# Performance work log

Hardware: AMD Instinct MI355X
Metric: run time of the kernel (lower is better)

Reference implementation:

```python
import jax, jax.numpy as jnp
import numpy as np

B, L, DM, DI, N = 8, 2048, 512, 768, 8  # batch, seq, d_model, d_inner=int(1.5*512), d_state


def setup_inputs() -> dict:
    key = jax.random.key(0)
    ks = jax.random.split(key, 8)
    g = lambda k, shape, sc=1.0: (jax.random.normal(k, shape, jnp.float32) * sc)
    return {
        "x": g(ks[0], (B, L, DM)),
        "W_in": g(ks[1], (DM, 2 * DI), 0.02),    # in_proj weight (stored in->out)
        "A_log": g(ks[2], (DI, N)),               # nn.Parameter(randn)
        "D_param": g(ks[3], (DI,)),               # skip-connection D
        "W_x": g(ks[4], (DI, N), 0.02),           # x_proj weight
        "W_dt": g(ks[5], (N, DI), 0.02),          # dt_proj weight
        "b_dt": jnp.zeros((DI,), jnp.float32),    # dt_proj bias
        "W_out": g(ks[6], (DI, DM), 0.02),        # out_proj weight
    }


def reference(x, W_in, A_log, D_param, W_x, W_dt, b_dt, W_out):
    xz = x @ W_in                                  # (B,L,2*DI)
    d_inner = W_in.shape[1] // 2
    x_ssm, z = xz[..., :d_inner], xz[..., d_inner:]
    x_ssm = jax.nn.silu(x_ssm)                     # (B,L,DI)
    A = -jnp.exp(A_log.astype(jnp.float32))        # (DI,N)
    delta = jax.nn.softplus((x_ssm @ W_x) @ W_dt + b_dt)  # (B,L,DI)

    n_state = A.shape[-1]

    def step(h, inp):
        xt, dt = inp                               # each (B,DI)
        dA = jnp.exp(dt[..., None] * A)            # (B,DI,N)
        h = dA * h + dt[..., None] * xt[..., None]
        y = jnp.sum(h, axis=-1) + D_param * xt     # (B,DI)
        return h, y

    h0 = jnp.zeros((x.shape[0], d_inner, n_state), x_ssm.dtype)
    xs = (jnp.swapaxes(x_ssm, 0, 1), jnp.swapaxes(delta, 0, 1))  # (L,B,DI)
    _, ys = jax.lax.scan(step, h0, xs)             # ys: (L,B,DI)
    y = jnp.swapaxes(ys, 0, 1)                     # (B,L,DI)
    y = y * jax.nn.silu(z)
    return y @ W_out                               # (B,L,DM)
```

## Files before the change

kernel.cpp:

```cpp
#include <hip/hip_runtime.h>

typedef unsigned short bfu;
typedef __attribute__((ext_vector_type(8))) short short8;
typedef __attribute__((ext_vector_type(4))) float f32x4;

__device__ __forceinline__ float bf2f(bfu u){
  union { unsigned int i; float f; } v; v.i = ((unsigned int)u) << 16; return v.f;
}
__device__ __forceinline__ bfu f2bf(float f){
  union { float f; unsigned int i; } v; v.f = f;
  unsigned int r = (v.i + 0x7FFFu + ((v.i >> 16) & 1u)) >> 16;
  return (bfu)r;
}
__device__ __forceinline__ float fexp2(float x){ return __builtin_amdgcn_exp2f(x); }
__device__ __forceinline__ float flog2(float x){ return __builtin_amdgcn_logf(x); }
__device__ __forceinline__ float softplusf(float x){
  float t = fexp2(-fabsf(x) * 1.44269504088896f);
  return fmaxf(x, 0.f) + 0.69314718055995f * flog2(1.f + t);
}
__device__ __forceinline__ void gload16(const bfu* g, bfu* l){
  __builtin_amdgcn_global_load_lds((const __attribute__((address_space(1))) unsigned int*)g,
                                   (__attribute__((address_space(3))) unsigned int*)l, 16, 0, 0);
}

__global__ __launch_bounds__(256) void cvt_all_kernel(const float* __restrict__ x, bfu* __restrict__ x_bf,
                                                      const float* __restrict__ W_in, const float* __restrict__ W_out,
                                                      const float* __restrict__ W_x,
                                                      bfu* __restrict__ WinT, bfu* __restrict__ WoutT,
                                                      float* __restrict__ WxT){
  __shared__ float T[32][33];
  const int bid = blockIdx.x;
  const int tid = threadIdx.x;
  if (bid < 8192){
    int g = bid * 256 + tid;
    float4 v = ((const float4*)x)[g];
    ushort4 o;
    o.x = f2bf(v.x); o.y = f2bf(v.y); o.z = f2bf(v.z); o.w = f2bf(v.w);
    ((ushort4*)x_bf)[g] = o;
    return;
  }
  const int lr = tid >> 3;
  const int lc = tid & 7;
  if (bid < 8960){
    int ti = bid - 8192;
    int r0 = (ti & 15) * 32, c0 = (ti >> 4) * 32;
    float4 v = *(const float4*)(W_in + (size_t)(r0 + lr) * 1536 + c0 + lc * 4);
    T[lr][lc * 4 + 0] = v.x; T[lr][lc * 4 + 1] = v.y;
    T[lr][lc * 4 + 2] = v.z; T[lr][lc * 4 + 3] = v.w;
    __syncthreads();
    ushort4 o;
    o.x = f2bf(T[lc * 4 + 0][lr]); o.y = f2bf(T[lc * 4 + 1][lr]);
    o.z = f2bf(T[lc * 4 + 2][lr]); o.w = f2bf(T[lc * 4 + 3][lr]);
    *(ushort4*)(WinT + (size_t)(c0 + lr) * 512 + r0 + lc * 4) = o;
  } else if (bid < 9344){
    int ti = bid - 8960;
    int r0 = (ti % 24) * 32, c0 = (ti / 24) * 32;
    float4 v = *(const float4*)(W_out + (size_t)(r0 + lr) * 512 + c0 + lc * 4);
    T[lr][lc * 4 + 0] = v.x; T[lr][lc * 4 + 1] = v.y;
    T[lr][lc * 4 + 2] = v.z; T[lr][lc * 4 + 3] = v.w;
    __syncthreads();
    ushort4 o;
    o.x = f2bf(T[lc * 4 + 0][lr]); o.y = f2bf(T[lc * 4 + 1][lr]);
    o.z = f2bf(T[lc * 4 + 2][lr]); o.w = f2bf(T[lc * 4 + 3][lr]);
    *(ushort4*)(WoutT + (size_t)(c0 + lr) * 768 + r0 + lc * 4) = o;
  } else {
    int h = (bid - 9344) * 256 + tid;
    int n = h / 768, k = h % 768;
    WxT[h] = W_x[(size_t)k * 8 + n];
  }
}

template<int EPI, int BM, int KK>
__global__ __launch_bounds__(BM * 2)
void gemm_sb(const bfu* __restrict__ Amat, const bfu* __restrict__ Bt,
             void* __restrict__ out0, void* __restrict__ out1,
             int NBN, int N)
{
  constexpr int BN = 128;
  constexpr int THREADS = BM * 2;
  constexpr int RPI = THREADS / 8;
  __shared__ bfu As[BM * 64];
  __shared__ bfu Bs[BN * 64];
  const int tid  = threadIdx.x;
  const int lane = tid & 63;
  const int w    = tid >> 6;
  const int wr   = w >> 1, wc = w & 1;

  const int cpx = gridDim.x >> 3;
  const int id  = blockIdx.x;
  const int nid = (id & 7) * cpx + (id >> 3);
  const int bn  = nid % NBN;
  const int bm  = nid / NBN;

  const int srow = tid >> 3;
  const int scol = ((tid & 7) ^ (srow & 7)) * 8;
  const bfu* gA = Amat + ((size_t)(bm * BM + srow)) * KK + scol;
  const bfu* gB = Bt   + ((size_t)(bn * BN + srow)) * KK + scol;
  bfu* lA = As + srow * 64 + (tid & 7) * 8;
  bfu* lB = Bs + srow * 64 + (tid & 7) * 8;

  f32x4 acc[4][4];
  #pragma unroll
  for (int i = 0; i < 4; i++)
    #pragma unroll
    for (int j = 0; j < 4; j++)
      #pragma unroll
      for (int r = 0; r < 4; r++) acc[i][j][r] = 0.f;

  for (int k0 = 0; k0 < KK; k0 += 64){
    #pragma unroll
    for (int i = 0; i < BM / RPI; i++)
      gload16(gA + (size_t)(i * RPI) * KK + k0, lA + i * RPI * 64);
    #pragma unroll
    for (int j = 0; j < BN / RPI; j++)
      gload16(gB + (size_t)(j * RPI) * KK + k0, lB + j * RPI * 64);
    __syncthreads();

    #pragma unroll
    for (int kk = 0; kk < 2; kk++){
      short8 a[4], b[4];
      const int sA = ((kk * 4 + (lane >> 4)) ^ (lane & 7)) * 8;
      #pragma unroll
      for (int m = 0; m < 4; m++){
        int r = wr * 64 + m * 16 + (lane & 15);
        a[m] = *(const short8*)&As[r * 64 + sA];
      }
      #pragma unroll
      for (int n = 0; n < 4; n++){
        int r = wc * 64 + n * 16 + (lane & 15);
        b[n] = *(const short8*)&Bs[r * 64 + sA];
      }
      #pragma unroll
      for (int m = 0; m < 4; m++)
        #pragma unroll
        for (int n = 0; n < 4; n++)
          acc[m][n] = __builtin_amdgcn_mfma_f32_16x16x32_bf16(a[m], b[n], acc[m][n], 0, 0, 0);
    }
    __syncthreads();
  }

  #pragma unroll
  for (int m = 0; m < 4; m++){
    #pragma unroll
    for (int n = 0; n < 4; n++){
      const int row0 = bm * BM + wr * 64 + m * 16 + (lane >> 4) * 4;
      const int col  = bn * BN + wc * 64 + n * 16 + (lane & 15);
      #pragma unroll
      for (int r = 0; r < 4; r++){
        float v = acc[m][n][r];
        int row = row0 + r;
        if (EPI == 0){
          float s = v / (1.f + __expf(-v));
          if (col < 768) ((bfu*)out0)[(size_t)row * 768 + col]         = f2bf(s);
          else           ((bfu*)out1)[(size_t)row * 768 + (col - 768)] = f2bf(s);
        } else {
          ((float*)out0)[(size_t)row * N + col] = v;
        }
      }
    }
  }
}

__global__ __launch_bounds__(256) void u_kernel(const bfu* __restrict__ xssm, const float* __restrict__ WxT,
                                                float* __restrict__ u){
  int wid = threadIdx.x >> 6, lane = threadIdx.x & 63;
  int row = blockIdx.x * 4 + wid;
  const bfu* xr = xssm + (size_t)row * 768;
  float acc[8];
  #pragma unroll
  for (int n = 0; n < 8; n++) acc[n] = 0.f;
  #pragma unroll
  for (int i = 0; i < 3; i++){
    int kb = i * 256 + lane * 4;
    ushort4 xq = *(const ushort4*)(xr + kb);
    float x0 = bf2f(xq.x), x1 = bf2f(xq.y), x2 = bf2f(xq.z), x3 = bf2f(xq.w);
    #pragma unroll
    for (int n = 0; n < 8; n++){
      float4 wv = *(const float4*)(WxT + (size_t)n * 768 + kb);
      acc[n] += x0 * wv.x + x1 * wv.y + x2 * wv.z + x3 * wv.w;
    }
  }
  #pragma unroll
  for (int n = 0; n < 8; n++){
    #pragma unroll
    for (int off = 32; off >= 1; off >>= 1) acc[n] += __shfl_xor(acc[n], off, 64);
  }
  if (lane == 0){
    float4 o0 = { acc[0], acc[1], acc[2], acc[3] };
    float4 o1 = { acc[4], acc[5], acc[6], acc[7] };
    *(float4*)(u + (size_t)row * 8)     = o0;
    *(float4*)(u + (size_t)row * 8 + 4) = o1;
  }
}

__global__ __launch_bounds__(256) void scan_phase1(const bfu* __restrict__ xssm, const float* __restrict__ u,
    const float* __restrict__ Wdt, const float* __restrict__ bdt, const float* __restrict__ A_log,
    float* __restrict__ Sws, float* __restrict__ Hws){
  __shared__ float uS[32][8];
  int tid = threadIdx.x;
  int bid = blockIdx.x;
  int b = bid / 192; int rem = bid % 192;
  int c = rem / 3;   int dblk = rem % 3;
  int d = dblk * 256 + tid;
  int r0 = b * 2048 + c * 32;
  uS[tid >> 3][tid & 7] = u[(size_t)(r0 + (tid >> 3)) * 8 + (tid & 7)];
  float Al2[8], H[8], Wr[8];
  float bd = bdt[d], S = 0.f;
  #pragma unroll
  for (int n = 0; n < 8; n++){
    Al2[n] = -__expf(A_log[(size_t)d * 8 + n]) * 1.4426950408889634f;
    Wr[n]  = Wdt[(size_t)n * 768 + d];
    H[n] = 0.f;
  }
  __syncthreads();
  size_t base = (size_t)r0 * 768 + d;
  #pragma unroll 8
  for (int i = 0; i < 32; i++){
    float4 u0 = *(const float4*)&uS[i][0];
    float4 u1 = *(const float4*)&uS[i][4];
    float xt = bf2f(xssm[base + (size_t)i * 768]);
    float dv = bd + u0.x * Wr[0] + u0.y * Wr[1] + u0.z * Wr[2] + u0.w * Wr[3]
                  + u1.x * Wr[4] + u1.y * Wr[5] + u1.z * Wr[6] + u1.w * Wr[7];
    float dt = softplusf(dv);
    float dx = dt * xt;
    S += dt;
    #pragma unroll
    for (int n = 0; n < 8; n++){
      float e = fexp2(dt * Al2[n]);
      H[n] = e * H[n] + dx;
    }
  }
  size_t o = (((size_t)b * 64 + c) * 768 + d) * 8;
  float4 h0 = { H[0], H[1], H[2], H[3] };
  float4 h1 = { H[4], H[5], H[6], H[7] };
  *(float4*)(Hws + o)     = h0;
  *(float4*)(Hws + o + 4) = h1;
  Sws[((size_t)b * 64 + c) * 768 + d] = S;
}

__global__ __launch_bounds__(256) void scan_phase2(const float* __restrict__ Sws, const float* __restrict__ Hws,
                                                   const float* __restrict__ A_log, float* __restrict__ Hin){
  int g = blockIdx.x * 256 + threadIdx.x;
  int within = g % 6144;
  int b = g / 6144;
  int d = within >> 3, n = within & 7;
  float Al2 = -__expf(A_log[(size_t)d * 8 + n]) * 1.4426950408889634f;
  size_t baseH = (size_t)b * 64 * 6144 + within;
  size_t baseS = (size_t)b * 64 * 768 + d;
  float hin = 0.f;
  float sv[16], hv[16];
  #pragma unroll
  for (int B = 0; B < 4; B++){
    #pragma unroll
    for (int i = 0; i < 16; i++){
      sv[i] = Sws[baseS + (size_t)(B * 16 + i) * 768];
      hv[i] = Hws[baseH + (size_t)(B * 16 + i) * 6144];
    }
    #pragma unroll
    for (int i = 0; i < 16; i++){
      size_t idx = baseH + (size_t)(B * 16 + i) * 6144;
      Hin[idx] = hin;
      hin = fexp2(sv[i] * Al2) * hin + hv[i];
    }
  }
}

__global__ __launch_bounds__(256) void scan_phase3(const bfu* __restrict__ xssm, const float* __restrict__ u,
    const float* __restrict__ Wdt, const float* __restrict__ bdt, const float* __restrict__ A_log,
    const float* __restrict__ Dp, const bfu* __restrict__ siluz, const float* __restrict__ Hin,
    bfu* __restrict__ yz){
  __shared__ float uS[32][8];
  int tid = threadIdx.x;
  int bid = blockIdx.x;
  int b = bid / 192; int rem = bid % 192;
  int c = rem / 3;   int dblk = rem % 3;
  int d = dblk * 256 + tid;
  int r0 = b * 2048 + c * 32;
  uS[tid >> 3][tid & 7] = u[(size_t)(r0 + (tid >> 3)) * 8 + (tid & 7)];
  float Al2[8], H[8], Wr[8];
  float bd = bdt[d], Dd = Dp[d];
  size_t o = (((size_t)b * 64 + c) * 768 + d) * 8;
  float4 h0 = *(const float4*)(Hin + o);
  float4 h1 = *(const float4*)(Hin + o + 4);
  H[0] = h0.x; H[1] = h0.y; H[2] = h0.z; H[3] = h0.w;
  H[4] = h1.x; H[5] = h1.y; H[6] = h1.z; H[7] = h1.w;
  #pragma unroll
  for (int n = 0; n < 8; n++){
    Al2[n] = -__expf(A_log[(size_t)d * 8 + n]) * 1.4426950408889634f;
    Wr[n]  = Wdt[(size_t)n * 768 + d];
  }
  __syncthreads();
  size_t base = (size_t)r0 * 768 + d;
  #pragma unroll 8
  for (int i = 0; i < 32; i++){
    float4 u0 = *(const float4*)&uS[i][0];
    float4 u1 = *(const float4*)&uS[i][4];
    float xt = bf2f(xssm[base + (size_t)i * 768]);
    float sz = bf2f(siluz[base + (size_t)i * 768]);
    float dv = bd + u0.x * Wr[0] + u0.y * Wr[1] + u0.z * Wr[2] + u0.w * Wr[3]
                  + u1.x * Wr[4] + u1.y * Wr[5] + u1.z * Wr[6] + u1.w * Wr[7];
    float dt = softplusf(dv);
    float dx = dt * xt;
    float y = Dd * xt;
    #pragma unroll
    for (int n = 0; n < 8; n++){
      float e = fexp2(dt * Al2[n]);
      H[n] = e * H[n] + dx;
      y += H[n];
    }
    yz[base + (size_t)i * 768] = f2bf(y * sz);
  }
}

extern "C" void kernel_launch(void* const* d_in, const int* in_sizes, int n_in,
                              void* d_out, int out_size, void* d_ws, size_t ws_size,
                              hipStream_t stream){
  const float* x     = (const float*)d_in[0];
  const float* W_in  = (const float*)d_in[1];
  const float* A_log = (const float*)d_in[2];
  const float* D_par = (const float*)d_in[3];
  const float* W_x   = (const float*)d_in[4];
  const float* W_dt  = (const float*)d_in[5];
  const float* b_dt  = (const float*)d_in[6];
  const float* W_out = (const float*)d_in[7];
  float* out = (float*)d_out;
  (void)in_sizes; (void)n_in; (void)out_size; (void)ws_size;

  char* base = (char*)d_ws;
  size_t off = 0;
  auto alloc = [&](size_t bytes)->char*{
    char* p = base + off; off += (bytes + 255) & ~(size_t)255; return p;
  };
  bfu*   x_bf  = (bfu*)  alloc((size_t)16384 * 512 * 2);
  bfu*   WinT  = (bfu*)  alloc((size_t)1536 * 512 * 2);
  bfu*   WoutT = (bfu*)  alloc((size_t)512 * 768 * 2);
  float* WxT   = (float*)alloc((size_t)8 * 768 * 4);
  bfu*   xssm  = (bfu*)  alloc((size_t)16384 * 768 * 2);
  bfu*   siluz = (bfu*)  alloc((size_t)16384 * 768 * 2);
  float* u     = (float*)alloc((size_t)16384 * 8 * 4);
  float* Sws   = (float*)alloc((size_t)8 * 64 * 768 * 4);
  float* Hws   = (float*)alloc((size_t)8 * 64 * 768 * 8 * 4);
  float* Hin   = (float*)alloc((size_t)8 * 64 * 768 * 8 * 4);
  bfu*   yz    = (bfu*)  alloc((size_t)16384 * 768 * 2);

  cvt_all_kernel<<<9368, 256, 0, stream>>>(x, x_bf, W_in, W_out, W_x, WinT, WoutT, WxT);
  gemm_sb<0, 256, 512><<<768, 512, 0, stream>>>(x_bf, WinT, xssm, siluz, 12, 1536);
  u_kernel<<<4096, 256, 0, stream>>>(xssm, WxT, u);
  scan_phase1<<<1536, 256, 0, stream>>>(xssm, u, W_dt, b_dt, A_log, Sws, Hws);
  scan_phase2<<<192, 256, 0, stream>>>(Sws, Hws, A_log, Hin);
  scan_phase3<<<1536, 256, 0, stream>>>(xssm, u, W_dt, b_dt, A_log, D_par, siluz, Hin, yz);
  gemm_sb<1, 128, 768><<<512, 256, 0, stream>>>(yz, WoutT, out, nullptr, 4, 512);
}
```

Before: 138.4 us.

## Add 256x256 ping-pong MFMA GEMM for in_proj with phased LDS pipelining

Adds a new bf16 GEMM kernel with 256x256 output tiles and 8 waves in a 2x4 layout. It double-buffers LDS and interleaves global-to-LDS loads with four MFMA phases per K-tile, separated by barriers and s_setprio. The in_proj GEMM uses it instead of the 256x128 kernel, halving the grid to 384 blocks. The goal is more A/B reuse and better overlap of loads with MFMA, at the cost of 128KB LDS per block (one block per CU) and heavy register use for the 8x4 accumulator tile.

After: 152.0 us. 1.1x slower.

```diff
diff --git a/kernel.cpp b/kernel.cpp
--- a/kernel.cpp
+++ b/kernel.cpp
@@ -70,6 +70,167 @@
   }
 }
 
+template<int EPI, int KK>
+__global__ __launch_bounds__(512)
+void gemm_8x(const bfu* __restrict__ Amat, const bfu* __restrict__ Bt,
+             void* __restrict__ out0, void* __restrict__ out1,
+             int NBN, int N)
+{
+  constexpr int NT = KK / 64;
+  __shared__ bfu LDS[4 * 16384];
+  const int tid  = threadIdx.x;
+  const int lane = tid & 63;
+  const int w    = tid >> 6;
+  const int wr   = w >> 2;
+  const int wc   = w & 3;
+
+  const int cpx = gridDim.x >> 3;
+  const int id  = blockIdx.x;
+  const int nid = (id & 7) * cpx + (id >> 3);
+  const int bn  = nid % NBN;
+  const int bm  = nid / NBN;
+
+  const int srow = tid >> 3;
+  const int scol = ((tid & 7) ^ (srow & 7)) * 8;
+  const bfu* gA = Amat + ((size_t)(bm * 256 + srow)) * KK + scol;
+  const bfu* gB = Bt   + ((size_t)(bn * 256 + srow)) * KK + scol;
+
+  auto stA = [&](int t, int q){
+    bfu* dst = (bfu*)LDS + (t & 1) * 16384 + q * 4096 + tid * 8;
+    gload16(gA + (size_t)(q * 64) * KK + t * 64, dst);
+  };
+  auto stB = [&](int t, int q){
+    bfu* dst = (bfu*)LDS + 32768 + (t & 1) * 16384 + q * 4096 + tid * 8;
+    gload16(gB + (size_t)(q * 64) * KK + t * 64, dst);
+  };
+
+  #define RDA(dst, Abase, m0)                                          \
+    _Pragma("unroll") for (int mi = 0; mi < 4; mi++)                   \
+    _Pragma("unroll") for (int kk = 0; kk < 2; kk++){                  \
+      int r_ = wr * 128 + ((m0) + mi) * 16 + (lane & 15);              \
+      int s_ = ((kk * 4 + (lane >> 4)) ^ (lane & 7)) * 8;              \
+      dst[mi][kk] = *(const short8*)&Abase[r_ * 64 + s_];              \
+    }
+  #define RDB(dst, Bbase, n0)                                          \
+    _Pragma("unroll") for (int ni = 0; ni < 2; ni++)                   \
+    _Pragma("unroll") for (int kk = 0; kk < 2; kk++){                  \
+      int r_ = wc * 64 + ((n0) + ni) * 16 + (lane & 15);               \
+      int s_ = ((kk * 4 + (lane >> 4)) ^ (lane & 7)) * 8;              \
+      dst[ni][kk] = *(const short8*)&Bbase[r_ * 64 + s_];              \
+    }
+  #define MM16(av, bv, m0, n0)                                         \
+    _Pragma("unroll") for (int mi = 0; mi < 4; mi++)                   \
+    _Pragma("unroll") for (int ni = 0; ni < 2; ni++)                   \
+    _Pragma("unroll") for (int kk = 0; kk < 2; kk++)                   \
+      acc[(m0) + mi][(n0) + ni] = __builtin_amdgcn_mfma_f32_16x16x32_bf16( \
+          av[mi][kk], bv[ni][kk], acc[(m0) + mi][(n0) + ni], 0, 0, 0);
+  #define PH_SYNC()                                                    \
+    __builtin_amdgcn_s_barrier();                                      \
+    asm volatile("s_waitcnt lgkmcnt(0)" ::: "memory");                 \
+    __builtin_amdgcn_sched_barrier(0);
+
+  f32x4 acc[8][4];
+  #pragma unroll
+  for (int i = 0; i < 8; i++)
+    #pragma unroll
+    for (int j = 0; j < 4; j++)
+      #pragma unroll
+      for (int r = 0; r < 4; r++) acc[i][j][r] = 0.f;
+
+  stA(0, 1); stA(0, 3);
+  stB(0, 0); stB(0, 1);
+  stB(0, 2); stB(0, 3);
+  stA(0, 0); stA(0, 2);
+  stA(1, 1); stA(1, 3);
+  stB(1, 0); stB(1, 1);
+  asm volatile("s_waitcnt vmcnt(4)" ::: "memory");
+  __builtin_amdgcn_s_barrier();
+
+  for (int t = 0; t < NT; t += 2){
+    const bfu* Ab0 = (const bfu*)LDS + (t & 1) * 16384;
+    const bfu* Bb0 = (const bfu*)LDS + 32768 + (t & 1) * 16384;
+    const bfu* Ab1 = (const bfu*)LDS + ((t + 1) & 1) * 16384;
+    const bfu* Bb1 = (const bfu*)LDS + 32768 + ((t + 1) & 1) * 16384;
+    short8 a[4][2], a2[4][2], b[2][2];
+
+    RDA(a, Ab0, 0); RDB(b, Bb0, 0);
+    stB(t + 1, 2); stB(t + 1, 3);
+    PH_SYNC();
+    __builtin_amdgcn_s_setprio(1); MM16(a, b, 0, 0); __builtin_amdgcn_s_setprio(0);
+    __builtin_amdgcn_s_barrier();
+
+    RDA(a2, Ab0, 4);
+    stA(t + 1, 0); stA(t + 1, 2);
+    PH_SYNC();
+    __builtin_amdgcn_s_setprio(1); MM16(a2, b, 4, 0); __builtin_amdgcn_s_setprio(0);
+    __builtin_amdgcn_s_barrier();
+
+    RDB(b, Bb0, 2);
+    if (t + 2 < NT){ stA(t + 2, 1); stA(t + 2, 3); }
+    PH_SYNC();
+    __builtin_amdgcn_s_setprio(1); MM16(a2, b, 4, 2); __builtin_amdgcn_s_setprio(0);
+    __builtin_amdgcn_s_barrier();
+
+    RDA(a, Ab0, 0);
+    if (t + 2 < NT){ stB(t + 2, 0); stB(t + 2, 1); }
+    PH_SYNC();
+    __builtin_amdgcn_s_setprio(1); MM16(a, b, 0, 2); __builtin_amdgcn_s_setprio(0);
+    if (t + 2 < NT) asm volatile("s_waitcnt vmcnt(4)" ::: "memory");
+    else            asm volatile("s_waitcnt vmcnt(0)" ::: "memory");
+    __builtin_amdgcn_s_barrier();
+
+    RDA(a, Ab1, 0); RDB(b, Bb1, 0);
+    if (t + 2 < NT){ stB(t + 2, 2); stB(t + 2, 3); }
+    PH_SYNC();
+    __builtin_amdgcn_s_setprio(1); MM16(a, b, 0, 0); __builtin_amdgcn_s_setprio(0);
+    __builtin_amdgcn_s_barrier();
+
+    RDA(a2, Ab1, 4);
+    if (t + 2 < NT){ stA(t + 2, 0); stA(t + 2, 2); }
+    PH_SYNC();
+    __builtin_amdgcn_s_setprio(1); MM16(a2, b, 4, 0); __builtin_amdgcn_s_setprio(0);
+    __builtin_amdgcn_s_barrier();
+
+    RDB(b, Bb1, 2);
+    if (t + 3 < NT){ stA(t + 3, 1); stA(t + 3, 3); }
+    PH_SYNC();
+    __builtin_amdgcn_s_setprio(1); MM16(a2, b, 4, 2); __builtin_amdgcn_s_setprio(0);
+    __builtin_amdgcn_s_barrier();
+
+    RDA(a, Ab1, 0);
+    if (t + 3 < NT){ stB(t + 3, 0); stB(t + 3, 1); }
+    PH_SYNC();
+    __builtin_amdgcn_s_setprio(1); MM16(a, b, 0, 2); __builtin_amdgcn_s_setprio(0);
+    asm volatile("s_waitcnt vmcnt(4)" ::: "memory");
+    __builtin_amdgcn_s_barrier();
+  }
+  #undef RDA
+  #undef RDB
+  #undef MM16
+  #undef PH_SYNC
+
+  #pragma unroll
+  for (int m = 0; m < 8; m++){
+    #pragma unroll
+    for (int n = 0; n < 4; n++){
+      const int row0 = bm * 256 + wr * 128 + m * 16 + (lane >> 4) * 4;
+      const int col  = bn * 256 + wc * 64 + n * 16 + (lane & 15);
+      #pragma unroll
+      for (int r = 0; r < 4; r++){
+        float v = acc[m][n][r];
+        int row = row0 + r;
+        if (EPI == 0){
+          float s = v / (1.f + __expf(-v));
+          if (col < 768) ((bfu*)out0)[(size_t)row * 768 + col]         = f2bf(s);
+          else           ((bfu*)out1)[(size_t)row * 768 + (col - 768)] = f2bf(s);
+        } else {
+          ((float*)out0)[(size_t)row * N + col] = v;
+        }
+      }
+    }
+  }
+}
+
 template<int EPI, int BM, int KK>
 __global__ __launch_bounds__(BM * 2)
 void gemm_sb(const bfu* __restrict__ Amat, const bfu* __restrict__ Bt,
@@ -344,7 +505,7 @@
   bfu*   yz    = (bfu*)  alloc((size_t)16384 * 768 * 2);
 
   cvt_all_kernel<<<9368, 256, 0, stream>>>(x, x_bf, W_in, W_out, W_x, WinT, WoutT, WxT);
-  gemm_sb<0, 256, 512><<<768, 512, 0, stream>>>(x_bf, WinT, xssm, siluz, 12, 1536);
+  gemm_8x<0, 512><<<384, 512, 0, stream>>>(x_bf, WinT, xssm, siluz, 6, 1536);
   u_kernel<<<4096, 256, 0, stream>>>(xssm, WxT, u);
   scan_phase1<<<1536, 256, 0, stream>>>(xssm, u, W_dt, b_dt, A_log, Sws, Hws);
   scan_phase2<<<192, 256, 0, stream>>>(Sws, Hws, A_log, Hin);
```
